# Optimization experiments

Hardware: AMD Instinct MI355X
Metric: run time of the kernel (lower is better)

The kernel has to match this reference:

```python
import jax, jax.numpy as jnp
import numpy as np

B, N, IN_DIM, HID, OUT, HEADS = 2, 1024, 64, 64, 64, 4
PHD1, PHD2 = HID // HEADS, OUT // HEADS
SLOPE = 0.2  # PyG GATv2Conv default negative_slope
EPS = 1e-12  # F.normalize eps


def _gatv2_dense(x, Wl, Wr, att, bias, heads, phd, mask):
    """Dense GATv2 layer over a full adjacency mask.
    x: [B,N,Din]; Wl/Wr: [Din, heads*phd]; att: [heads,phd]; bias: [heads*phd];
    mask: [N,N] bool, mask[i,j]=True means edge j->i exists.
    """
    Bb, Nn, _ = x.shape
    xl = (x @ Wl).reshape(Bb, Nn, heads, phd)  # source features
    xr = (x @ Wr).reshape(Bb, Nn, heads, phd)  # target features
    # s[b,i,j,h,p] = leaky_relu(xr[b,i] + xl[b,j])  (GATv2)
    s = jax.nn.leaky_relu(xr[:, :, None] + xl[:, None, :], SLOPE)
    e = jnp.einsum('bijhp,hp->bijh', s, att)  # [B,Ni,Nj,H]
    e = jnp.where(mask[None, :, :, None], e, -jnp.inf)
    alpha = jax.nn.softmax(e, axis=2)  # softmax over source nodes j
    out = jnp.einsum('bijh,bjhp->bihp', alpha, xl).reshape(Bb, Nn, heads * phd)
    return out + bias


def setup_inputs() -> dict:
    key = jax.random.key(0)
    ks = jax.random.split(key, 10)
    sc = 0.1
    return {
        'x': jax.random.normal(ks[0], (B, N, IN_DIM), jnp.float32),
        'embedding': jax.random.normal(ks[1], (N, HID), jnp.float32),
        'Wl1': jax.random.normal(ks[2], (IN_DIM, HEADS * PHD1), jnp.float32) * sc,
        'Wr1': jax.random.normal(ks[3], (IN_DIM, HEADS * PHD1), jnp.float32) * sc,
        'att1': jax.random.normal(ks[4], (HEADS, PHD1), jnp.float32) * sc,
        'b1': jnp.zeros((HEADS * PHD1,), jnp.float32),
        'Wl2': jax.random.normal(ks[5], (HID, HEADS * PHD2), jnp.float32) * sc,
        'Wr2': jax.random.normal(ks[6], (HID, HEADS * PHD2), jnp.float32) * sc,
        'att2': jax.random.normal(ks[7], (HEADS, PHD2), jnp.float32) * sc,
        'b2': jnp.zeros((HEADS * PHD2,), jnp.float32),
    }


def reference(x, embedding, Wl1, Wr1, att1, b1, Wl2, Wr2, att2, b2):
    # AdaptiveAdjacency: cosine-similarity adjacency; only its nonzero pattern is used.
    norm = jnp.maximum(jnp.linalg.norm(embedding, axis=1, keepdims=True), EPS)
    ne = embedding / norm
    adj = ne @ ne.T  # [N,N]
    # edge set = adj.nonzero(); GATv2Conv(add_self_loops=True) guarantees diagonal
    mask = (adj != 0) | jnp.eye(N, dtype=bool)
    h = jax.nn.relu(_gatv2_dense(x, Wl1, Wr1, att1, b1, HEADS, PHD1, mask))
    # dropout(0.3) in eval mode -> identity
    return _gatv2_dense(h, Wl2, Wr2, att2, b2, HEADS, PHD2, mask)
```

## Files before the change

kernel.cpp:

```cpp
#include <hip/hip_runtime.h>
#include <math.h>

#define NN 1024
#define BB 2
#define D 64
#define NHEAD 4
#define LOG2E 1.4426950408889634f
#define MST 65

template <int CTRL>
__device__ __forceinline__ float dpp_mov(float x) {
    int xi = __builtin_bit_cast(int, x);
    int r = __builtin_amdgcn_update_dpp(0, xi, CTRL, 0xF, 0xF, true);
    return __builtin_bit_cast(float, r);
}

__device__ __forceinline__ float dpp_rowsum16(float t) {
    t += dpp_mov<0x111>(t);
    t += dpp_mov<0x112>(t);
    t += dpp_mov<0x114>(t);
    t += dpp_mov<0x118>(t);
    return t;
}

__global__ __launch_bounds__(256) void k_mask_gemm(
    const float* __restrict__ emb, unsigned char* __restrict__ mask,
    const float* __restrict__ A, const float* __restrict__ Wl,
    const float* __restrict__ Wr, const float* __restrict__ att,
    float* __restrict__ xl, float* __restrict__ xr, float* __restrict__ alE)
{
    __shared__ float SH[64 * MST * 2];
    int tid = threadIdx.x;
    if (blockIdx.x < 256) {
        float* As = SH;
        float* Bs = SH + 64 * MST;
        int ib = (blockIdx.x & 15) << 6;
        int jb = (blockIdx.x >> 4) << 6;

        #pragma unroll
        for (int r = 0; r < 4; ++r) {
            int q = tid + (r << 8);
            int row = q >> 4, c4 = (q & 15) << 2;
            float4 a = *(const float4*)&emb[(ib + row) * D + c4];
            float4 b = *(const float4*)&emb[(jb + row) * D + c4];
            As[row * MST + c4 + 0] = a.x; As[row * MST + c4 + 1] = a.y;
            As[row * MST + c4 + 2] = a.z; As[row * MST + c4 + 3] = a.w;
            Bs[row * MST + c4 + 0] = b.x; Bs[row * MST + c4 + 1] = b.y;
            Bs[row * MST + c4 + 2] = b.z; Bs[row * MST + c4 + 3] = b.w;
        }
        __syncthreads();

        int i0 = (tid >> 4) << 2;
        int j0 = (tid & 15) << 2;
        float acc[4][4] = {};
        #pragma unroll 8
        for (int k = 0; k < 64; ++k) {
            float a0 = As[(i0 + 0) * MST + k];
            float a1 = As[(i0 + 1) * MST + k];
            float a2 = As[(i0 + 2) * MST + k];
            float a3 = As[(i0 + 3) * MST + k];
            float b0 = Bs[(j0 + 0) * MST + k];
            float b1 = Bs[(j0 + 1) * MST + k];
            float b2 = Bs[(j0 + 2) * MST + k];
            float b3 = Bs[(j0 + 3) * MST + k];
            acc[0][0] = fmaf(a0, b0, acc[0][0]); acc[0][1] = fmaf(a0, b1, acc[0][1]);
            acc[0][2] = fmaf(a0, b2, acc[0][2]); acc[0][3] = fmaf(a0, b3, acc[0][3]);
            acc[1][0] = fmaf(a1, b0, acc[1][0]); acc[1][1] = fmaf(a1, b1, acc[1][1]);
            acc[1][2] = fmaf(a1, b2, acc[1][2]); acc[1][3] = fmaf(a1, b3, acc[1][3]);
            acc[2][0] = fmaf(a2, b0, acc[2][0]); acc[2][1] = fmaf(a2, b1, acc[2][1]);
            acc[2][2] = fmaf(a2, b2, acc[2][2]); acc[2][3] = fmaf(a2, b3, acc[2][3]);
            acc[3][0] = fmaf(a3, b0, acc[3][0]); acc[3][1] = fmaf(a3, b1, acc[3][1]);
            acc[3][2] = fmaf(a3, b2, acc[3][2]); acc[3][3] = fmaf(a3, b3, acc[3][3]);
        }
        #pragma unroll
        for (int r = 0; r < 4; ++r) {
            int gi = ib + i0 + r;
            uchar4 m;
            m.x = (acc[r][0] != 0.f || gi == jb + j0 + 0) ? 1 : 0;
            m.y = (acc[r][1] != 0.f || gi == jb + j0 + 1) ? 1 : 0;
            m.z = (acc[r][2] != 0.f || gi == jb + j0 + 2) ? 1 : 0;
            m.w = (acc[r][3] != 0.f || gi == jb + j0 + 3) ? 1 : 0;
            *(uchar4*)&mask[gi * NN + jb + j0] = m;
        }
    } else {
        float* wl = SH;
        float* wr = SH + 4096;
        for (int t = tid; t < 4096; t += 256) { wl[t] = Wl[t]; wr[t] = Wr[t]; }
        __syncthreads();
        int r = (blockIdx.x - 256) * 4 + (tid >> 6);
        int c = tid & 63;
        float av = att[c];
        const float* arow = A + r * 64;
        float accl = 0.f, accr = 0.f;
        #pragma unroll
        for (int p = 0; p < 64; ++p) {
            float a = arow[p];
            accl = fmaf(a, wl[p * 64 + c], accl);
            accr = fmaf(a, wr[p * 64 + c], accr);
        }
        int cp = (((c >> 2) & 3) << 4) | ((c >> 4) << 2) | (c & 3);
        xl[r * 64 + cp] = accl;
        xr[r * 64 + c] = accr;
        float t = dpp_rowsum16(accl * av);
        if ((c & 15) == 15) alE[(r << 2) | (c >> 4)] = 0.6f * LOG2E * t;
    }
}

template <bool RELU, bool FUSEG>
__global__ __launch_bounds__(256, 2) void k_attn(
    const float* __restrict__ xlp, const float* __restrict__ xr,
    const float* __restrict__ att, const float* __restrict__ alE,
    const float* __restrict__ bias, const unsigned char* __restrict__ mask,
    float* __restrict__ out,
    const float* __restrict__ Wl2, const float* __restrict__ Wr2,
    const float* __restrict__ att2,
    float* __restrict__ xl2, float* __restrict__ xr2, float* __restrict__ alE2)
{
    __shared__ float Opart[4][4][4][64];
    __shared__ float Lpart[4][4][4][NHEAD];
    __shared__ float SHW[FUSEG ? 8192 : 1];
    __shared__ float RES[FUSEG ? 4 : 1][64];

    int tid = threadIdx.x;
    int wave = tid >> 6, lane = tid & 63;
    int h = lane & 3, jl = lane >> 2;
    int b = blockIdx.x >> 8;
    int i0 = (blockIdx.x & 255) << 2;
    int j0 = (wave << 8) + (jl << 4);

    if constexpr (FUSEG) {
        for (int t = tid; t < 4096; t += 256) { SHW[t] = Wl2[t]; SHW[4096 + t] = Wr2[t]; }
    }

    const float* xlb = xlp + (b << 16);

    float at[16], xr0f[16], xr1f[16], xr2f[16], xr3f[16];
    {
        const float* ap = att + (h << 4);
        const float* r0 = xr + (((b << 10) + i0) << 6) + (h << 4);
        const float* r1 = r0 + 64;
        const float* r2 = r0 + 128;
        const float* r3 = r0 + 192;
        #pragma unroll
        for (int c = 0; c < 4; ++c) {
            *(float4*)&at[c << 2]   = *(const float4*)(ap + (c << 2));
            *(float4*)&xr0f[c << 2] = *(const float4*)(r0 + (c << 2));
            *(float4*)&xr1f[c << 2] = *(const float4*)(r1 + (c << 2));
            *(float4*)&xr2f[c << 2] = *(const float4*)(r2 + (c << 2));
            *(float4*)&xr3f[c << 2] = *(const float4*)(r3 + (c << 2));
        }
        #pragma unroll
        for (int p = 0; p < 16; ++p) at[p] *= 0.4f * LOG2E;
    }
    float ar0, ar1, ar2, ar3;
    {
        float s0[4], s1[4], s2[4], s3[4];
        #pragma unroll
        for (int c = 0; c < 4; ++c) {
            float t0 = 0.f, t1 = 0.f, t2 = 0.f, t3 = 0.f;
            #pragma unroll
            for (int r = 0; r < 4; ++r) {
                int p = (c << 2) + r;
                float a = at[p];
                t0 = fmaf(a, xr0f[p], t0);
                t1 = fmaf(a, xr1f[p], t1);
                t2 = fmaf(a, xr2f[p], t2);
                t3 = fmaf(a, xr3f[p], t3);
            }
            s0[c] = t0; s1[c] = t1; s2[c] = t2; s3[c] = t3;
        }
        ar0 = 1.5f * ((s0[0] + s0[1]) + (s0[2] + s0[3]));
        ar1 = 1.5f * ((s1[0] + s1[1]) + (s1[2] + s1[3]));
        ar2 = 1.5f * ((s2[0] + s2[1]) + (s2[2] + s2[3]));
        ar3 = 1.5f * ((s3[0] + s3[1]) + (s3[2] + s3[3]));
    }

    unsigned mb0 = 0, mb1 = 0, mb2 = 0, mb3 = 0;
    {
        const unsigned* m0p = (const unsigned*)(mask + (i0 + 0) * NN + j0);
        const unsigned* m1p = (const unsigned*)(mask + (i0 + 1) * NN + j0);
        const unsigned* m2p = (const unsigned*)(mask + (i0 + 2) * NN + j0);
        const unsigned* m3p = (const unsigned*)(mask + (i0 + 3) * NN + j0);
        #pragma unroll
        for (int q = 0; q < 4; ++q) {
            unsigned w0 = m0p[q], w1 = m1p[q], w2 = m2p[q], w3 = m3p[q];
            mb0 |= ((((w0 >> 0) & 1) | ((w0 >> 7) & 2) | ((w0 >> 14) & 4) | ((w0 >> 21) & 8)) << (q << 2));
            mb1 |= ((((w1 >> 0) & 1) | ((w1 >> 7) & 2) | ((w1 >> 14) & 4) | ((w1 >> 21) & 8)) << (q << 2));
            mb2 |= ((((w2 >> 0) & 1) | ((w2 >> 7) & 2) | ((w2 >> 14) & 4) | ((w2 >> 21) & 8)) << (q << 2));
            mb3 |= ((((w3 >> 0) & 1) | ((w3 >> 7) & 2) | ((w3 >> 14) & 4) | ((w3 >> 21) & 8)) << (q << 2));
        }
    }

    float O0[16], O1[16], O2[16], O3[16];
    float lq0 = 0.f, lq1 = 0.f, lq2 = 0.f, lq3 = 0.f;
    #pragma unroll
    for (int p = 0; p < 16; ++p) { O0[p] = 0.f; O1[p] = 0.f; O2[p] = 0.f; O3[p] = 0.f; }

    const float* xrow = xlb + (j0 << 6) + (h << 2);
    const float* alp  = alE + (b << 12) + (j0 << 2) + h;

    #pragma unroll 2
    for (int s = 0; s < 16; ++s) {
        const float* rp = xrow + (s << 6);
        float xv[16];
        *(float4*)&xv[0]  = *(const float4*)(rp);
        *(float4*)&xv[4]  = *(const float4*)(rp + 16);
        *(float4*)&xv[8]  = *(const float4*)(rp + 32);
        *(float4*)&xv[12] = *(const float4*)(rp + 48);
        float alr = alp[s << 2];
        bool m0 = (mb0 >> s) & 1, m1 = (mb1 >> s) & 1;
        bool m2 = (mb2 >> s) & 1, m3 = (mb3 >> s) & 1;

        float s0[4], s1[4], s2[4], s3[4];
        #pragma unroll
        for (int c = 0; c < 4; ++c) {
            float t0 = 0.f, t1 = 0.f, t2 = 0.f, t3 = 0.f;
            #pragma unroll
            for (int r = 0; r < 4; ++r) {
                int p = (c << 2) + r;
                float a = at[p], xvv = xv[p];
                t0 = fmaf(a, __builtin_fabsf(xr0f[p] + xvv), t0);
                t1 = fmaf(a, __builtin_fabsf(xr1f[p] + xvv), t1);
                t2 = fmaf(a, __builtin_fabsf(xr2f[p] + xvv), t2);
                t3 = fmaf(a, __builtin_fabsf(xr3f[p] + xvv), t3);
            }
            s0[c] = t0; s1[c] = t1; s2[c] = t2; s3[c] = t3;
        }
        float e0 = ((s0[0] + s0[1]) + (s0[2] + s0[3])) + (ar0 + alr);
        float e1 = ((s1[0] + s1[1]) + (s1[2] + s1[3])) + (ar1 + alr);
        float e2 = ((s2[0] + s2[1]) + (s2[2] + s2[3])) + (ar2 + alr);
        float e3 = ((s3[0] + s3[1]) + (s3[2] + s3[3])) + (ar3 + alr);
        float pe0 = m0 ? __builtin_amdgcn_exp2f(e0) : 0.f;
        float pe1 = m1 ? __builtin_amdgcn_exp2f(e1) : 0.f;
        float pe2 = m2 ? __builtin_amdgcn_exp2f(e2) : 0.f;
        float pe3 = m3 ? __builtin_amdgcn_exp2f(e3) : 0.f;
        lq0 += pe0; lq1 += pe1; lq2 += pe2; lq3 += pe3;
        #pragma unroll
        for (int p = 0; p < 16; ++p) {
            float xvv = xv[p];
            O0[p] = fmaf(pe0, xvv, O0[p]);
            O1[p] = fmaf(pe1, xvv, O1[p]);
            O2[p] = fmaf(pe2, xvv, O2[p]);
            O3[p] = fmaf(pe3, xvv, O3[p]);
        }
    }

    #pragma unroll
    for (int p = 0; p < 16; ++p) {
        O0[p] += dpp_mov<0x114>(O0[p]);  O0[p] += dpp_mov<0x118>(O0[p]);
        O1[p] += dpp_mov<0x114>(O1[p]);  O1[p] += dpp_mov<0x118>(O1[p]);
        O2[p] += dpp_mov<0x114>(O2[p]);  O2[p] += dpp_mov<0x118>(O2[p]);
        O3[p] += dpp_mov<0x114>(O3[p]);  O3[p] += dpp_mov<0x118>(O3[p]);
    }
    lq0 += dpp_mov<0x114>(lq0);  lq0 += dpp_mov<0x118>(lq0);
    lq1 += dpp_mov<0x114>(lq1);  lq1 += dpp_mov<0x118>(lq1);
    lq2 += dpp_mov<0x114>(lq2);  lq2 += dpp_mov<0x118>(lq2);
    lq3 += dpp_mov<0x114>(lq3);  lq3 += dpp_mov<0x118>(lq3);

    if ((lane & 15) >= 12) {
        int k = lane >> 4;
        #pragma unroll
        for (int c = 0; c < 4; ++c) {
            *(float4*)&Opart[0][wave][k][(h << 4) + (c << 2)] = *(const float4*)&O0[c << 2];
            *(float4*)&Opart[1][wave][k][(h << 4) + (c << 2)] = *(const float4*)&O1[c << 2];
            *(float4*)&Opart[2][wave][k][(h << 4) + (c << 2)] = *(const float4*)&O2[c << 2];
            *(float4*)&Opart[3][wave][k][(h << 4) + (c << 2)] = *(const float4*)&O3[c << 2];
        }
        Lpart[0][wave][k][h] = lq0;
        Lpart[1][wave][k][h] = lq1;
        Lpart[2][wave][k][h] = lq2;
        Lpart[3][wave][k][h] = lq3;
    }
    __syncthreads();

    {
        int ii = tid >> 6, c = tid & 63;
        float o = 0.f, l = 0.f;
        #pragma unroll
        for (int w = 0; w < 4; ++w)
            #pragma unroll
            for (int k = 0; k < 4; ++k) {
                o += Opart[ii][w][k][c];
                l += Lpart[ii][w][k][c >> 4];
            }
        float res = o / l + bias[c];
        if (RELU) res = fmaxf(res, 0.f);
        if constexpr (FUSEG) {
            RES[ii][c] = res;
        } else {
            out[((b << 10) + i0 + ii) * D + c] = res;
        }
    }

    if constexpr (FUSEG) {
        __syncthreads();
        int ii = tid >> 6, c = tid & 63;
        int rr = (blockIdx.x << 2) + ii;
        float av = att2[c];
        const float* arow = &RES[ii][0];
        float accl = 0.f, accr = 0.f;
        #pragma unroll
        for (int p = 0; p < 64; ++p) {
            float a = arow[p];
            accl = fmaf(a, SHW[p * 64 + c], accl);
            accr = fmaf(a, SHW[4096 + p * 64 + c], accr);
        }
        int cp = (((c >> 2) & 3) << 4) | ((c >> 4) << 2) | (c & 3);
        xl2[rr * 64 + cp] = accl;
        xr2[rr * 64 + c] = accr;
        float t = dpp_rowsum16(accl * av);
        if ((c & 15) == 15) alE2[(rr << 2) | (c >> 4)] = 0.6f * LOG2E * t;
    }
}

extern "C" void kernel_launch(void* const* d_in, const int* in_sizes, int n_in,
                              void* d_out, int out_size, void* d_ws, size_t ws_size,
                              hipStream_t stream) {
    const float* x    = (const float*)d_in[0];
    const float* emb  = (const float*)d_in[1];
    const float* Wl1  = (const float*)d_in[2];
    const float* Wr1  = (const float*)d_in[3];
    const float* att1 = (const float*)d_in[4];
    const float* b1   = (const float*)d_in[5];
    const float* Wl2  = (const float*)d_in[6];
    const float* Wr2  = (const float*)d_in[7];
    const float* att2 = (const float*)d_in[8];
    const float* b2   = (const float*)d_in[9];
    float* out = (float*)d_out;

    unsigned char* mask = (unsigned char*)d_ws;
    float* xl   = (float*)(mask + NN * NN);
    float* xr   = xl + BB * NN * D;
    float* xl2  = xr + BB * NN * D;
    float* alE  = xl2 + BB * NN * D;
    float* xr2  = alE + BB * NN * NHEAD;
    float* alE2 = xr2 + BB * NN * D;

    k_mask_gemm<<<256 + BB * NN / 4, 256, 0, stream>>>(emb, mask, x, Wl1, Wr1, att1, xl, xr, alE);

    k_attn<true, true><<<BB * NN / 4, 256, 0, stream>>>(
        xl, xr, att1, alE, b1, mask, xl2 ,
        Wl2, Wr2, att2, xl2, xr2, alE2);

    k_attn<false, false><<<BB * NN / 4, 256, 0, stream>>>(
        xl2, xr2, att2, alE2, b2, mask, out,
        Wl2, Wr2, att2, xl2, xr2, alE2 );
}
```

Before: 128.2 us.

## Stage xl tiles through double-buffered swizzled LDS with coalesced loads

The attention kernel now loads each wave's 1024-float xl tile per step with fully coalesced float4 global loads into a double-buffered, XOR-swizzled LDS region, then reads per-lane rows from LDS. This replaces the earlier strided per-lane global reads and prefetches two steps ahead. The mask bit gathering is rewritten to use byte loads plus DPP OR-reductions, and the weight buffer now reuses the same LDS after the loop. The goal is better global coalescing, at the cost of extra LDS traffic, register pressure and a possible change in occupancy. The mapping from j to lanes also changes to j = wave*256 + s*16 + jl.

```diff
diff --git a/kernel.cpp b/kernel.cpp
--- a/kernel.cpp
+++ b/kernel.cpp
@@ -13,6 +13,11 @@
     int xi = __builtin_bit_cast(int, x);
     int r = __builtin_amdgcn_update_dpp(0, xi, CTRL, 0xF, 0xF, true);
     return __builtin_bit_cast(float, r);
+}
+template <int CTRL>
+__device__ __forceinline__ unsigned dpp_movi(unsigned x) {
+    int r = __builtin_amdgcn_update_dpp(0, (int)x, CTRL, 0xF, 0xF, true);
+    return (unsigned)r;
 }
 
 __device__ __forceinline__ float dpp_rowsum16(float t) {
@@ -116,21 +121,16 @@
     const float* __restrict__ att2,
     float* __restrict__ xl2, float* __restrict__ xr2, float* __restrict__ alE2)
 {
+    __shared__ __align__(16) float XS[8192];
     __shared__ float Opart[4][4][4][64];
     __shared__ float Lpart[4][4][4][NHEAD];
-    __shared__ float SHW[FUSEG ? 8192 : 1];
-    __shared__ float RES[FUSEG ? 4 : 1][64];
+    __shared__ float RES[4][64];
 
     int tid = threadIdx.x;
     int wave = tid >> 6, lane = tid & 63;
     int h = lane & 3, jl = lane >> 2;
     int b = blockIdx.x >> 8;
     int i0 = (blockIdx.x & 255) << 2;
-    int j0 = (wave << 8) + (jl << 4);
-
-    if constexpr (FUSEG) {
-        for (int t = tid; t < 4096; t += 256) { SHW[t] = Wl2[t]; SHW[4096 + t] = Wr2[t]; }
-    }
 
     const float* xlb = xlp + (b << 16);
 
@@ -175,20 +175,28 @@
         ar3 = 1.5f * ((s3[0] + s3[1]) + (s3[2] + s3[3]));
     }
 
-    unsigned mb0 = 0, mb1 = 0, mb2 = 0, mb3 = 0;
-    {
-        const unsigned* m0p = (const unsigned*)(mask + (i0 + 0) * NN + j0);
-        const unsigned* m1p = (const unsigned*)(mask + (i0 + 1) * NN + j0);
-        const unsigned* m2p = (const unsigned*)(mask + (i0 + 2) * NN + j0);
-        const unsigned* m3p = (const unsigned*)(mask + (i0 + 3) * NN + j0);
-        #pragma unroll
-        for (int q = 0; q < 4; ++q) {
-            unsigned w0 = m0p[q], w1 = m1p[q], w2 = m2p[q], w3 = m3p[q];
-            mb0 |= ((((w0 >> 0) & 1) | ((w0 >> 7) & 2) | ((w0 >> 14) & 4) | ((w0 >> 21) & 8)) << (q << 2));
-            mb1 |= ((((w1 >> 0) & 1) | ((w1 >> 7) & 2) | ((w1 >> 14) & 4) | ((w1 >> 21) & 8)) << (q << 2));
-            mb2 |= ((((w2 >> 0) & 1) | ((w2 >> 7) & 2) | ((w2 >> 14) & 4) | ((w2 >> 21) & 8)) << (q << 2));
-            mb3 |= ((((w3 >> 0) & 1) | ((w3 >> 7) & 2) | ((w3 >> 14) & 4) | ((w3 >> 21) & 8)) << (q << 2));
-        }
+    unsigned mb0, mb1, mb2, mb3;
+    {
+        const unsigned char* mp = mask + i0 * NN + (wave << 8) + jl;
+        int hh = h << 6;
+        unsigned n0 = (unsigned)mp[hh] | ((unsigned)mp[hh + 16] << 1)
+                    | ((unsigned)mp[hh + 32] << 2) | ((unsigned)mp[hh + 48] << 3);
+        mp += NN;
+        unsigned n1 = (unsigned)mp[hh] | ((unsigned)mp[hh + 16] << 1)
+                    | ((unsigned)mp[hh + 32] << 2) | ((unsigned)mp[hh + 48] << 3);
+        mp += NN;
+        unsigned n2 = (unsigned)mp[hh] | ((unsigned)mp[hh + 16] << 1)
+                    | ((unsigned)mp[hh + 32] << 2) | ((unsigned)mp[hh + 48] << 3);
+        mp += NN;
+        unsigned n3 = (unsigned)mp[hh] | ((unsigned)mp[hh + 16] << 1)
+                    | ((unsigned)mp[hh + 32] << 2) | ((unsigned)mp[hh + 48] << 3);
+        unsigned v0 = n0 << (h << 2), v1 = n1 << (h << 2);
+        unsigned v2 = n2 << (h << 2), v3 = n3 << (h << 2);
+        v0 |= dpp_movi<0xB1>(v0); v0 |= dpp_movi<0x4E>(v0);
+        v1 |= dpp_movi<0xB1>(v1); v1 |= dpp_movi<0x4E>(v1);
+        v2 |= dpp_movi<0xB1>(v2); v2 |= dpp_movi<0x4E>(v2);
+        v3 |= dpp_movi<0xB1>(v3); v3 |= dpp_movi<0x4E>(v3);
+        mb0 = v0; mb1 = v1; mb2 = v2; mb3 = v3;
     }
 
     float O0[16], O1[16], O2[16], O3[16];
@@ -196,18 +204,49 @@
     #pragma unroll
     for (int p = 0; p < 16; ++p) { O0[p] = 0.f; O1[p] = 0.f; O2[p] = 0.f; O3[p] = 0.f; }
 
-    const float* xrow = xlb + (j0 << 6) + (h << 2);
-    const float* alp  = alE + (b << 12) + (j0 << 2) + h;
+    const float* tb = xlb + (wave << 14);
+    float* XB = XS + (wave << 11);
+    int l4 = lane << 2;
+    int rowoff = (lane >> 4) << 6;
+    int sb = (lane & 15) ^ (lane >> 4);
+    int A0 = rowoff + (sb << 2);
+    int A1 = rowoff + ((sb ^ 4) << 2);
+    int qx = (jl >> 2) & 1;
+    int rb = (jl << 6) + ((h ^ (jl & 3)) << 2);
+    const float* alp = alE + (b << 12) + (wave << 10) + lane;
+
+    float4 ga, gb, gc, gd;
+    {
+        const float* p = tb + l4;
+        ga = *(const float4*)p;       gb = *(const float4*)(p + 256);
+        gc = *(const float4*)(p + 512); gd = *(const float4*)(p + 768);
+        *(float4*)&XB[A0] = ga;         *(float4*)&XB[256 + A1] = gb;
+        *(float4*)&XB[512 + A0] = gc;   *(float4*)&XB[768 + A1] = gd;
+        p = tb + 1024 + l4;
+        ga = *(const float4*)p;       gb = *(const float4*)(p + 256);
+        gc = *(const float4*)(p + 512); gd = *(const float4*)(p + 768);
+    }
 
     #pragma unroll 2
     for (int s = 0; s < 16; ++s) {
-        const float* rp = xrow + (s << 6);
+        if (s < 15) {
+            float* w = XB + (((s + 1) & 1) << 10);
+            *(float4*)&w[A0] = ga;         *(float4*)&w[256 + A1] = gb;
+            *(float4*)&w[512 + A0] = gc;   *(float4*)&w[768 + A1] = gd;
+        }
+        if (s < 14) {
+            const float* p = tb + ((s + 2) << 10) + l4;
+            ga = *(const float4*)p;       gb = *(const float4*)(p + 256);
+            gc = *(const float4*)(p + 512); gd = *(const float4*)(p + 768);
+        }
+
+        const float* XBr = XB + ((s & 1) << 10);
         float xv[16];
-        *(float4*)&xv[0]  = *(const float4*)(rp);
-        *(float4*)&xv[4]  = *(const float4*)(rp + 16);
-        *(float4*)&xv[8]  = *(const float4*)(rp + 32);
-        *(float4*)&xv[12] = *(const float4*)(rp + 48);
-        float alr = alp[s << 2];
+        *(float4*)&xv[0]  = *(const float4*)&XBr[rb + (((0 ^ qx)) << 4)];
+        *(float4*)&xv[4]  = *(const float4*)&XBr[rb + (((1 ^ qx)) << 4)];
+        *(float4*)&xv[8]  = *(const float4*)&XBr[rb + (((2 ^ qx)) << 4)];
+        *(float4*)&xv[12] = *(const float4*)&XBr[rb + (((3 ^ qx)) << 4)];
+        float alr = alp[s << 6];
         bool m0 = (mb0 >> s) & 1, m1 = (mb1 >> s) & 1;
         bool m2 = (mb2 >> s) & 1, m3 = (mb3 >> s) & 1;
 
@@ -245,6 +284,11 @@
         }
     }
 
+    if constexpr (FUSEG) {
+        __syncthreads();
+        for (int t = tid; t < 4096; t += 256) { XS[t] = Wl2[t]; XS[4096 + t] = Wr2[t]; }
+    }
+
     #pragma unroll
     for (int p = 0; p < 16; ++p) {
         O0[p] += dpp_mov<0x114>(O0[p]);  O0[p] += dpp_mov<0x118>(O0[p]);
@@ -302,8 +346,8 @@
         #pragma unroll
         for (int p = 0; p < 64; ++p) {
             float a = arow[p];
-            accl = fmaf(a, SHW[p * 64 + c], accl);
-            accr = fmaf(a, SHW[4096 + p * 64 + c], accr);
+            accl = fmaf(a, XS[p * 64 + c], accl);
+            accr = fmaf(a, XS[4096 + p * 64 + c], accr);
         }
         int cp = (((c >> 2) & 3) << 4) | ((c >> 4) << 2) | (c & 3);
         xl2[rr * 64 + cp] = accl;
```

Measured after the change: 121.3 us. 5.4% less time.
